# Performance work log

Hardware: AMD Instinct MI355X
Metric: run time of the kernel (lower is better)

## Reference

```python
import jax, jax.numpy as jnp
import numpy as np
import math

B, S, D = 2, 2048, 2048
H = 16
DK = D // H


def build_rotary(dim, seq_len):
    inv_freq = 1.0 / (10000.0 ** (np.arange(0, dim, 2, dtype=np.float32) / dim))
    t = np.arange(seq_len, dtype=np.float32)
    freqs = np.einsum('i,j->ij', t, inv_freq)
    emb = np.concatenate([freqs, freqs], axis=-1)  # [S, dim]
    return jnp.asarray(np.cos(emb))[None, None], jnp.asarray(np.sin(emb))[None, None]


def rotate_half(x):
    x1, x2 = jnp.split(x, 2, axis=-1)
    return jnp.concatenate([-x2, x1], axis=-1)


def setup_inputs() -> dict:
    key = jax.random.key(0)
    ks = jax.random.split(key, 12)
    s = 1.0 / math.sqrt(D)
    inp = {
        'query': jax.random.normal(ks[0], (B, S, D), jnp.float32),
        'key': jax.random.normal(ks[1], (B, S, D), jnp.float32),
        'value': jax.random.normal(ks[2], (B, S, D), jnp.float32),
        'mask': jnp.tril(jnp.ones((S, S), bool))[None, None],  # causal [1,1,S,S]
        'wq': jax.random.uniform(ks[3], (D, D), jnp.float32, -s, s),
        'bq': jax.random.uniform(ks[4], (D,), jnp.float32, -s, s),
        'wk': jax.random.uniform(ks[5], (D, D), jnp.float32, -s, s),
        'bk': jax.random.uniform(ks[6], (D,), jnp.float32, -s, s),
        'wv': jax.random.uniform(ks[7], (D, D), jnp.float32, -s, s),
        'bv': jax.random.uniform(ks[8], (D,), jnp.float32, -s, s),
        'wo': jax.random.uniform(ks[9], (D, D), jnp.float32, -s, s),
        'bo': jax.random.uniform(ks[10], (D,), jnp.float32, -s, s),
    }
    return inp


def reference(query, key, value, mask, wq, bq, wk, bk, wv, bv, wo, bo):
    Bc, Sc, _ = query.shape
    # QKV projections -> [B, H, S, DK]
    def proj(x, w, b):
        return (x @ w.T + b).reshape(Bc, Sc, H, DK).transpose(0, 2, 1, 3)
    q = proj(query, wq, bq)
    k = proj(key, wk, bk)
    v = proj(value, wv, bv)
    # inline RoPE
    cos, sin = build_rotary(DK, Sc)
    cos = cos.astype(query.dtype)
    sin = sin.astype(query.dtype)
    q = q * cos + rotate_half(q) * sin
    k = k * cos + rotate_half(k) * sin
    # attention (dropout in eval / identity)
    scores = jnp.einsum('bhqd,bhkd->bhqk', q, k) / math.sqrt(DK)
    scores = jnp.where(mask, scores.astype(jnp.float32), -1e9)
    p = jax.nn.softmax(scores, axis=-1)
    x = jnp.einsum('bhqk,bhkd->bhqd', p, v)
    x = x.transpose(0, 2, 1, 3).reshape(Bc, Sc, H * DK)
    return x @ wo.T + bo
```

## Files before the change

### kernel.cpp

```cpp
#include <hip/hip_runtime.h>
#include <hip/hip_bf16.h>

#define Bc 2
#define Sc 2048
#define Dc 2048
#define Hc 16
#define DKc 128
#define Mc (Bc * Sc)
#define Kc Dc
#define Nc Dc
#define NX ((size_t)Bc * Sc * Dc)
#define NW ((size_t)Dc * Dc)
#define NTK (Kc / 32)

#define SM_C 0.1275174366f

typedef unsigned short u16;
using bf16x8  = __bf16 __attribute__((ext_vector_type(8)));
using ushort8 = unsigned short __attribute__((ext_vector_type(8)));
using ushort4v = unsigned short __attribute__((ext_vector_type(4)));
using floatx4 = float __attribute__((ext_vector_type(4)));
using float4v = float __attribute__((ext_vector_type(4)));

__device__ __forceinline__ u16 f2bf(float f) {
  union { float f; unsigned u; } x; x.f = f;
  unsigned r = x.u + 0x7fffu + ((x.u >> 16) & 1u);
  return (u16)(r >> 16);
}
__device__ __forceinline__ float bf2f(u16 u) {
  union { unsigned u; float f; } x; x.u = ((unsigned)u) << 16;
  return x.f;
}
__device__ __forceinline__ bf16x8 load8(const u16* p) {
  return __builtin_bit_cast(bf16x8, *(const ushort8*)p);
}
__device__ __forceinline__ floatx4 mfma16(bf16x8 a, bf16x8 b, floatx4 c) {
  return __builtin_amdgcn_mfma_f32_16x16x32_bf16(a, b, c, 0, 0, 0);
}
__device__ __forceinline__ void async16(const void* g, void* l) {
  __builtin_amdgcn_global_load_lds(
      (__attribute__((address_space(1))) void*)(g),
      (__attribute__((address_space(3))) void*)(l), 16, 0, 0);
}

__global__ __launch_bounds__(256) void cast_all(
    const float* __restrict__ q, const float* __restrict__ k,
    const float* __restrict__ v, const float* __restrict__ wq,
    const float* __restrict__ wk, const float* __restrict__ wv,
    const float* __restrict__ wo, u16* __restrict__ dst) {
  size_t i4 = (size_t)blockIdx.x * 256 + threadIdx.x;
  size_t e = i4 * 4;
  const float* src; size_t off;
  if (e < 3 * NX) {
    size_t w = e / NX;
    src = (w == 0) ? q : (w == 1) ? k : v;
    off = e - w * NX;
  } else {
    size_t e2 = e - 3 * NX;
    size_t w = e2 / NW;
    src = (w == 0) ? wq : (w == 1) ? wk : (w == 2) ? wv : wo;
    off = e2 - w * NW;
  }
  float4v val = *(const float4v*)(src + off);
  ushort4v o;
  o.x = f2bf(val.x); o.y = f2bf(val.y); o.z = f2bf(val.z); o.w = f2bf(val.w);
  *(ushort4v*)(dst + e) = o;
}

__device__ __forceinline__ void gemm_body(
    const u16* __restrict__ A, const u16* __restrict__ W,
    const float* __restrict__ bias, u16* __restrict__ out_bf,
    float* __restrict__ out_f, int epi, int m0, int n0,
    u16* __restrict__ lds ) {
  const int tid = threadIdx.x;
  const int wid = tid >> 6, lane = tid & 63;
  const int l15 = lane & 15, quad = lane >> 4;
  const int wm = wid >> 1, wn = wid & 1;

  const int sr = tid >> 2;
  const int sc = ((tid & 3) ^ ((tid >> 3) & 3)) * 8;
  const u16* gA = A + (size_t)(m0 + sr) * Kc + sc;
  const u16* gB = W + (size_t)(n0 + sr) * Kc + sc;
  const size_t half = (size_t)64 * Kc;

  const int slot8 = (quad ^ ((l15 >> 1) & 3)) * 8;
  const int arow0 = (wm * 64 + l15) * 32 + slot8;
  const int brow0 = 4096 + (wn * 64 + l15) * 32 + slot8;

  floatx4 acc[4][4] = {};

  u16* b0 = lds;
  u16* b1 = lds + 8192;
  u16* b2 = lds + 16384;

  async16(gA,             b0 + tid * 8);
  async16(gA + half,      b0 + 2048 + tid * 8);
  async16(gB,             b0 + 4096 + tid * 8);
  async16(gB + half,      b0 + 6144 + tid * 8);
  async16(gA + 32,        b1 + tid * 8);
  async16(gA + 32 + half, b1 + 2048 + tid * 8);
  async16(gB + 32,        b1 + 4096 + tid * 8);
  async16(gB + 32 + half, b1 + 6144 + tid * 8);
  asm volatile("s_waitcnt vmcnt(4)" ::: "memory");
  __builtin_amdgcn_s_barrier();

  const u16* gAt = gA + 64;
  const u16* gBt = gB + 64;

  for (int t = 0; t < NTK; ++t) {
    if (t < NTK - 2) {
      async16(gAt,        b2 + tid * 8);
      async16(gAt + half, b2 + 2048 + tid * 8);
      async16(gBt,        b2 + 4096 + tid * 8);
      async16(gBt + half, b2 + 6144 + tid * 8);
    }

    bf16x8 af[4], bfr[4];
#pragma unroll
    for (int m = 0; m < 4; ++m) af[m] = load8(b0 + arow0 + m * 512);
#pragma unroll
    for (int n = 0; n < 4; ++n) bfr[n] = load8(b0 + brow0 + n * 512);

    __builtin_amdgcn_s_setprio(1);
#pragma unroll
    for (int m = 0; m < 4; ++m)
#pragma unroll
      for (int n = 0; n < 4; ++n)
        acc[m][n] = mfma16(af[m], bfr[n], acc[m][n]);
    __builtin_amdgcn_s_setprio(0);

    if (t < NTK - 2)       asm volatile("s_waitcnt vmcnt(4)" ::: "memory");
    else if (t == NTK - 2) asm volatile("s_waitcnt vmcnt(0)" ::: "memory");
    __builtin_amdgcn_s_barrier();

    u16* tmp = b0; b0 = b1; b1 = b2; b2 = tmp;
    gAt += 32; gBt += 32;
  }

#pragma unroll
  for (int n = 0; n < 4; ++n) {
    int col = n0 + wn * 64 + n * 16 + l15;
    float bv = bias[col];
#pragma unroll
    for (int m = 0; m < 4; ++m) {
      int rowb = m0 + wm * 64 + m * 16 + quad * 4;
#pragma unroll
      for (int r = 0; r < 4; ++r) {
        float v = acc[m][n][r] + bv;
        int row = rowb + r;
        if (epi == 2) {
          out_f[(size_t)row * Nc + col] = v;
        } else {
          int b = row >> 11, s = row & 2047;
          int h = col >> 7, dk = col & 127;
          size_t addr = (epi == 0)
              ? ((size_t)(b * Hc + h) * Sc + s) * DKc + dk
              : ((size_t)(b * Hc + h) * DKc + dk) * Sc + s;
          out_bf[addr] = f2bf(v);
        }
      }
    }
  }
}

__global__ __launch_bounds__(256, 3) void gemm_qkv(
    const u16* __restrict__ xq, const u16* __restrict__ xk,
    const u16* __restrict__ xv, const u16* __restrict__ wcat,
    const float* __restrict__ bq, const float* __restrict__ bk,
    const float* __restrict__ bv, u16* __restrict__ qhw,
    u16* __restrict__ khw, u16* __restrict__ vtw) {
  __shared__ u16 lds[3 * 8192];
  const int proj = blockIdx.z;
  const int n0 = blockIdx.x * 128;
  const int m0 = blockIdx.y * 128;
  const u16* A = (proj == 0) ? xq : (proj == 1) ? xk : xv;
  const u16* W = wcat + (size_t)proj * 2048 * Kc;
  const float* bias = (proj == 0) ? bq : (proj == 1) ? bk : bv;
  u16* outp = (proj == 0) ? qhw : (proj == 1) ? khw : vtw;
  gemm_body(A, W, bias, outp, nullptr, (proj == 2) ? 1 : 0, m0, n0, lds);
}

__global__ __launch_bounds__(256, 3) void gemm_out(
    const u16* __restrict__ A, const u16* __restrict__ W,
    const float* __restrict__ bias, float* __restrict__ out_f) {
  __shared__ u16 lds[3 * 8192];
  gemm_body(A, W, bias, nullptr, out_f, 2, blockIdx.y * 128,
            blockIdx.x * 128, lds);
}

__global__ __launch_bounds__(256) void rope_kernel(u16* __restrict__ q,
                                                   u16* __restrict__ k) {
  int i = blockIdx.x * 256 + threadIdx.x;
  int d = i & 63;
  int s = (i >> 6) & (Sc - 1);
  int bh = i >> 17;
  size_t base = ((size_t)bh * Sc + s) * DKc;
  float inv_freq = exp2f((float)d * (-13.287712379549449f / 64.0f));
  float ang = (float)s * inv_freq;
  float sn, cs;
  sincosf(ang, &sn, &cs);
  float q1 = bf2f(q[base + d]), q2 = bf2f(q[base + d + 64]);
  q[base + d]      = f2bf((q1 * cs - q2 * sn) * SM_C);
  q[base + d + 64] = f2bf((q2 * cs + q1 * sn) * SM_C);
  float k1 = bf2f(k[base + d]), k2 = bf2f(k[base + d + 64]);
  k[base + d]      = f2bf(k1 * cs - k2 * sn);
  k[base + d + 64] = f2bf(k2 * cs + k1 * sn);
}

__global__ __launch_bounds__(256) void attn_kernel(
    const u16* __restrict__ qh, const u16* __restrict__ kh,
    const u16* __restrict__ vt, u16* __restrict__ ao) {
  __shared__ u16 Ksl[128 * 128];
  __shared__ u16 Vsl[144 * 128];
  const int tid = threadIdx.x;
  const int wid = tid >> 6, lane = tid & 63;
  const int l15 = lane & 15, quad = lane >> 4;
  const int qt = (blockIdx.z == 0) ? 15 - (int)blockIdx.x : (int)blockIdx.x;
  const int h = blockIdx.y, bb = blockIdx.z;
  const int bh = bb * Hc + h;
  const int q0 = qt * 128;
  const u16* qbase = qh + (size_t)bh * Sc * DKc;
  const u16* kbase = kh + (size_t)bh * Sc * DKc;
  const u16* vbase = vt + (size_t)bh * DKc * Sc;

  const int srow = tid >> 4;
  const int scol = (tid & 15) * 8;
  const int sdst = ((tid & 15) ^ srow) * 8;

  {
    int r = 128 + srow;
    u16 val = (r == 128) ? (u16)0x3F80 : (u16)0;
#pragma unroll
    for (int j = 0; j < 8; j++) Vsl[r * 128 + scol + j] = val;
  }

  bf16x8 qf[2][4];
#pragma unroll
  for (int mt = 0; mt < 2; mt++)
#pragma unroll
    for (int kq = 0; kq < 4; kq++)
      qf[mt][kq] = load8(qbase + (size_t)(q0 + wid * 32 + mt * 16 + l15) * DKc +
                         kq * 32 + quad * 8);

  floatx4 accO[2][9] = {};

  ushort8 kr[8], vr[8];
#pragma unroll
  for (int c = 0; c < 8; c++) {
    int rr = c * 16 + srow;
    kr[c] = *(const ushort8*)(kbase + (size_t)rr * DKc + scol);
    vr[c] = *(const ushort8*)(vbase + (size_t)rr * Sc + scol);
  }

  for (int kt = 0; kt <= qt; kt++) {
    __syncthreads();
#pragma unroll
    for (int c = 0; c < 8; c++) {
      int rr = c * 16 + srow;
      *(ushort8*)&Ksl[rr * 128 + sdst] = kr[c];
    }
    __syncthreads();

    floatx4 sacc[2][8] = {};
    __builtin_amdgcn_s_setprio(1);
#pragma unroll
    for (int kk = 0; kk < 4; kk++) {
      const int sb = ((kk * 4 + quad) ^ l15) * 8;
#pragma unroll
      for (int nt = 0; nt < 8; nt++) {
        bf16x8 kf = load8(&Ksl[(nt * 16 + l15) * 128 + sb]);
        sacc[0][nt] = mfma16(qf[0][kk], kf, sacc[0][nt]);
        sacc[1][nt] = mfma16(qf[1][kk], kf, sacc[1][nt]);
      }
    }
    __builtin_amdgcn_s_setprio(0);

#pragma unroll
    for (int c = 0; c < 8; c++) {
      int rr = c * 16 + srow;
      *(ushort8*)&Vsl[rr * 128 + sdst] = vr[c];
    }

    if (kt == qt) {
#pragma unroll
      for (int nt = 0; nt < 8; nt++) {
        int kcol = nt * 16 + l15;
#pragma unroll
        for (int mt = 0; mt < 2; mt++) {
          int qrow = wid * 32 + mt * 16 + quad * 4;
#pragma unroll
          for (int r = 0; r < 4; r++)
            if (kcol > qrow + r) sacc[mt][nt][r] = -1e30f;
        }
      }
    }

#pragma unroll
    for (int mt = 0; mt < 2; mt++)
#pragma unroll
      for (int nt = 0; nt < 8; nt++)
#pragma unroll
        for (int r = 0; r < 4; r++)
          sacc[mt][nt][r] = exp2f(sacc[mt][nt][r]);

    __syncthreads();

    u16* Pw = &Ksl[wid * 4096];
#pragma unroll
    for (int mt = 0; mt < 2; mt++)
#pragma unroll
      for (int nt = 0; nt < 8; nt++)
#pragma unroll
        for (int r = 0; r < 4; r++) {
          int row = mt * 16 + quad * 4 + r;
          int col = nt * 16 + l15;
          int sb = (col >> 3) ^ (row & 15);
          Pw[row * 128 + sb * 8 + (col & 7)] = f2bf(sacc[mt][nt][r]);
        }

    if (kt < qt) {
      const u16* kb = kbase + (size_t)(kt + 1) * 128 * DKc;
#pragma unroll
      for (int c = 0; c < 8; c++) {
        int rr = c * 16 + srow;
        kr[c] = *(const ushort8*)(kb + (size_t)rr * DKc + scol);
        vr[c] = *(const ushort8*)(vbase + (size_t)rr * Sc + (kt + 1) * 128 + scol);
      }
    }

    __builtin_amdgcn_s_setprio(1);
#pragma unroll
    for (int kk = 0; kk < 4; kk++) {
      const int sb = ((kk * 4 + quad) ^ l15) * 8;
      bf16x8 pf0 = load8(&Pw[(0 * 16 + l15) * 128 + sb]);
      bf16x8 pf1 = load8(&Pw[(1 * 16 + l15) * 128 + sb]);
#pragma unroll
      for (int nt = 0; nt < 9; nt++) {
        bf16x8 vf = load8(&Vsl[(nt * 16 + l15) * 128 + sb]);
        accO[0][nt] = mfma16(pf0, vf, accO[0][nt]);
        accO[1][nt] = mfma16(pf1, vf, accO[1][nt]);
      }
    }
    __builtin_amdgcn_s_setprio(0);
  }

#pragma unroll
  for (int mt = 0; mt < 2; mt++)
#pragma unroll
    for (int r = 0; r < 4; r++) {
      float lsum = __shfl(accO[mt][8][r], lane & 48);
      float inv = 1.0f / lsum;
      int gq = q0 + wid * 32 + mt * 16 + quad * 4 + r;
      size_t rowbase = ((size_t)bb * Sc + gq) * Dc + h * DKc;
#pragma unroll
      for (int nt = 0; nt < 8; nt++)
        ao[rowbase + nt * 16 + l15] = f2bf(accO[mt][nt][r] * inv);
    }
}

extern "C" void kernel_launch(void* const* d_in, const int* in_sizes, int n_in,
                              void* d_out, int out_size, void* d_ws,
                              size_t ws_size, hipStream_t stream) {
  const float* q  = (const float*)d_in[0];
  const float* k  = (const float*)d_in[1];
  const float* v  = (const float*)d_in[2];
  const float* wq = (const float*)d_in[4];
  const float* bq = (const float*)d_in[5];
  const float* wk = (const float*)d_in[6];
  const float* bk = (const float*)d_in[7];
  const float* wv = (const float*)d_in[8];
  const float* bv = (const float*)d_in[9];
  const float* wo = (const float*)d_in[10];
  const float* bo = (const float*)d_in[11];
  float* out = (float*)d_out;

  u16* ws = (u16*)d_ws;
  u16* xq  = ws;
  u16* xk  = ws + NX;
  u16* xv  = ws + 2 * NX;
  u16* wcat = ws + 3 * NX;
  u16* wob = ws + 3 * NX + 3 * NW;
  u16* qhw = ws + 3 * NX + 4 * NW;
  u16* khw = ws + 4 * NX + 4 * NW;
  u16* vtw = ws + 5 * NX + 4 * NW;
  u16* aow = ws + 6 * NX + 4 * NW;

  {
    size_t tot4 = (3 * NX + 4 * NW) / 4;
    cast_all<<<dim3((unsigned)(tot4 / 256)), 256, 0, stream>>>(
        q, k, v, wq, wk, wv, wo, ws);
  }
  gemm_qkv<<<dim3(Nc / 128, Mc / 128, 3), 256, 0, stream>>>(
      xq, xk, xv, wcat, bq, bk, bv, qhw, khw, vtw);
  rope_kernel<<<dim3(Bc * Hc * Sc * 64 / 256), 256, 0, stream>>>(qhw, khw);
  attn_kernel<<<dim3(Sc / 128, Hc, Bc), 256, 0, stream>>>(qhw, khw, vtw, aow);
  gemm_out<<<dim3(Nc / 128, Mc / 128), 256, 0, stream>>>(aow, wob, bo, out);
}
```

Before: 509.2 us.

## Keep softmax probabilities in registers via transposed QK MFMA and lane shuffles

Swaps the MFMA operand order so the score accumulators come out transposed, which lets the exponentiated P tile be packed to bf16 with v_cvt_pk and redistributed to the PV MFMA A-operand layout through cross-lane shuffles. The per-warp LDS round trip for P goes away, along with one __syncthreads per iteration. V is now written to LDS together with K before the first barrier. The cost is many ds_bpermute shuffles and extra registers for the packed values, and the new layout must map exactly onto the MFMA operand format to stay correct.

```diff
diff --git a/kernel.cpp b/kernel.cpp
--- a/kernel.cpp
+++ b/kernel.cpp
@@ -19,6 +19,7 @@
 using bf16x8  = __bf16 __attribute__((ext_vector_type(8)));
 using ushort8 = unsigned short __attribute__((ext_vector_type(8)));
 using ushort4v = unsigned short __attribute__((ext_vector_type(4)));
+using uint4v  = unsigned __attribute__((ext_vector_type(4)));
 using floatx4 = float __attribute__((ext_vector_type(4)));
 using float4v = float __attribute__((ext_vector_type(4)));
 
@@ -36,6 +37,11 @@
 }
 __device__ __forceinline__ floatx4 mfma16(bf16x8 a, bf16x8 b, floatx4 c) {
   return __builtin_amdgcn_mfma_f32_16x16x32_bf16(a, b, c, 0, 0, 0);
+}
+__device__ __forceinline__ unsigned cvt_pk(float lo, float hi) {
+  unsigned r;
+  asm("v_cvt_pk_bf16_f32 %0, %1, %2" : "=v"(r) : "v"(lo), "v"(hi));
+  return r;
 }
 __device__ __forceinline__ void async16(const void* g, void* l) {
   __builtin_amdgcn_global_load_lds(
@@ -252,12 +258,16 @@
     vr[c] = *(const ushort8*)(vbase + (size_t)rr * Sc + scol);
   }
 
+  const int srcb = l15 + ((quad & 1) << 5);
+  const bool hi2 = (quad >> 1) != 0;
+
   for (int kt = 0; kt <= qt; kt++) {
     __syncthreads();
 #pragma unroll
     for (int c = 0; c < 8; c++) {
       int rr = c * 16 + srow;
       *(ushort8*)&Ksl[rr * 128 + sdst] = kr[c];
+      *(ushort8*)&Vsl[rr * 128 + sdst] = vr[c];
     }
     __syncthreads();
 
@@ -269,54 +279,38 @@
 #pragma unroll
       for (int nt = 0; nt < 8; nt++) {
         bf16x8 kf = load8(&Ksl[(nt * 16 + l15) * 128 + sb]);
-        sacc[0][nt] = mfma16(qf[0][kk], kf, sacc[0][nt]);
-        sacc[1][nt] = mfma16(qf[1][kk], kf, sacc[1][nt]);
+        sacc[0][nt] = mfma16(kf, qf[0][kk], sacc[0][nt]);
+        sacc[1][nt] = mfma16(kf, qf[1][kk], sacc[1][nt]);
       }
     }
     __builtin_amdgcn_s_setprio(0);
 
-#pragma unroll
-    for (int c = 0; c < 8; c++) {
-      int rr = c * 16 + srow;
-      *(ushort8*)&Vsl[rr * 128 + sdst] = vr[c];
-    }
-
     if (kt == qt) {
 #pragma unroll
+      for (int nt = 0; nt < 8; nt++)
+#pragma unroll
+        for (int mt = 0; mt < 2; mt++) {
+          int qrow = wid * 32 + mt * 16 + l15;
+#pragma unroll
+          for (int r = 0; r < 4; r++) {
+            int kcol = nt * 16 + quad * 4 + r;
+            if (kcol > qrow) sacc[mt][nt][r] = -1e30f;
+          }
+        }
+    }
+
+    unsigned cpk[2][8][2];
+#pragma unroll
+    for (int mt = 0; mt < 2; mt++)
+#pragma unroll
       for (int nt = 0; nt < 8; nt++) {
-        int kcol = nt * 16 + l15;
-#pragma unroll
-        for (int mt = 0; mt < 2; mt++) {
-          int qrow = wid * 32 + mt * 16 + quad * 4;
-#pragma unroll
-          for (int r = 0; r < 4; r++)
-            if (kcol > qrow + r) sacc[mt][nt][r] = -1e30f;
-        }
-      }
-    }
-
-#pragma unroll
-    for (int mt = 0; mt < 2; mt++)
-#pragma unroll
-      for (int nt = 0; nt < 8; nt++)
-#pragma unroll
-        for (int r = 0; r < 4; r++)
-          sacc[mt][nt][r] = exp2f(sacc[mt][nt][r]);
-
-    __syncthreads();
-
-    u16* Pw = &Ksl[wid * 4096];
-#pragma unroll
-    for (int mt = 0; mt < 2; mt++)
-#pragma unroll
-      for (int nt = 0; nt < 8; nt++)
-#pragma unroll
-        for (int r = 0; r < 4; r++) {
-          int row = mt * 16 + quad * 4 + r;
-          int col = nt * 16 + l15;
-          int sb = (col >> 3) ^ (row & 15);
-          Pw[row * 128 + sb * 8 + (col & 7)] = f2bf(sacc[mt][nt][r]);
-        }
+        float e0 = exp2f(sacc[mt][nt][0]);
+        float e1 = exp2f(sacc[mt][nt][1]);
+        float e2 = exp2f(sacc[mt][nt][2]);
+        float e3 = exp2f(sacc[mt][nt][3]);
+        cpk[mt][nt][0] = cvt_pk(e0, e1);
+        cpk[mt][nt][1] = cvt_pk(e2, e3);
+      }
 
     if (kt < qt) {
       const u16* kb = kbase + (size_t)(kt + 1) * 128 * DKc;
@@ -328,20 +322,36 @@
       }
     }
 
-    __builtin_amdgcn_s_setprio(1);
 #pragma unroll
     for (int kk = 0; kk < 4; kk++) {
       const int sb = ((kk * 4 + quad) ^ l15) * 8;
-      bf16x8 pf0 = load8(&Pw[(0 * 16 + l15) * 128 + sb]);
-      bf16x8 pf1 = load8(&Pw[(1 * 16 + l15) * 128 + sb]);
+      bf16x8 pa[2];
+#pragma unroll
+      for (int mt = 0; mt < 2; mt++) {
+        unsigned a0 = __shfl(cpk[mt][2 * kk][0],     srcb);
+        unsigned a1 = __shfl(cpk[mt][2 * kk][1],     srcb);
+        unsigned a2 = __shfl(cpk[mt][2 * kk][0],     srcb + 16);
+        unsigned a3 = __shfl(cpk[mt][2 * kk][1],     srcb + 16);
+        unsigned b0 = __shfl(cpk[mt][2 * kk + 1][0], srcb);
+        unsigned b1 = __shfl(cpk[mt][2 * kk + 1][1], srcb);
+        unsigned b2 = __shfl(cpk[mt][2 * kk + 1][0], srcb + 16);
+        unsigned b3 = __shfl(cpk[mt][2 * kk + 1][1], srcb + 16);
+        uint4v uw;
+        uw.x = hi2 ? b0 : a0;
+        uw.y = hi2 ? b1 : a1;
+        uw.z = hi2 ? b2 : a2;
+        uw.w = hi2 ? b3 : a3;
+        pa[mt] = __builtin_bit_cast(bf16x8, uw);
+      }
+      __builtin_amdgcn_s_setprio(1);
 #pragma unroll
       for (int nt = 0; nt < 9; nt++) {
         bf16x8 vf = load8(&Vsl[(nt * 16 + l15) * 128 + sb]);
-        accO[0][nt] = mfma16(pf0, vf, accO[0][nt]);
-        accO[1][nt] = mfma16(pf1, vf, accO[1][nt]);
-      }
-    }
-    __builtin_amdgcn_s_setprio(0);
+        accO[0][nt] = mfma16(pa[0], vf, accO[0][nt]);
+        accO[1][nt] = mfma16(pa[1], vf, accO[1][nt]);
+      }
+      __builtin_amdgcn_s_setprio(0);
+    }
   }
 
 #pragma unroll
```

New measurement: 513.1 us. No clear change (+0.8%).
